# Performance work log

Hardware: AMD Instinct MI355X
Metric: run time of the kernel (lower is better)

The kernel has to match this reference:

```python
import jax, jax.numpy as jnp
import numpy as np

FACTOR = 5      # ProbAttention sampling factor
NHEAD = 8
LN_EPS = 1e-5


def pos_encoding(L, d):
    pos = np.arange(L, dtype=np.float32)[:, None]
    div = np.exp(np.arange(0, d, 2, dtype=np.float32) * (-np.log(10000.0) / d))
    pe = np.zeros((L, d), np.float32)
    pe[:, 0::2] = np.sin(pos * div)
    pe[:, 1::2] = np.cos(pos * div)
    return jnp.asarray(pe)


def layer_norm(x, s, b):
    mu = x.mean(-1, keepdims=True)
    var = ((x - mu) ** 2).mean(-1, keepdims=True)
    return (x - mu) * jax.lax.rsqrt(var + LN_EPS) * s + b


def prob_attention(x4, key):
    # x4: [B, L, H, D]; self-attention (Q=K=V=x4), mask_flag=False
    B, L, H, D = x4.shape
    q = jnp.transpose(x4, (0, 2, 1, 3))  # [B,H,L,D]
    u = max(1, min(FACTOR * int(np.ceil(np.log(L))), L))  # L_Q == L_K
    # random K-sampling: per-query random subset of keys (shared across B,H)
    idx = jax.random.randint(key, (L, u), 0, L)
    k_s = q[:, :, idx, :]                                # [B,H,L,u,D] irregular gather
    qk_s = jnp.einsum('bhld,bhlsd->bhls', q, k_s)        # [B,H,L,u]
    M = qk_s.max(-1) - qk_s.sum(-1) / L                  # sparsity measure
    _, top = jax.lax.top_k(M, u)                         # [B,H,u] active queries
    q_red = jnp.take_along_axis(q, top[..., None], axis=2)   # [B,H,u,D]
    scale = 1.0 / jnp.sqrt(jnp.float32(D))
    scores = jnp.einsum('bhud,bhkd->bhuk', q_red, q) * scale  # reduced-query scores
    attn = jax.nn.softmax(scores, axis=-1)
    ctx_top = jnp.einsum('bhuk,bhkd->bhud', attn, q)     # V == q here
    # initial context = mean of V (mask_flag=False), scatter top-query results
    ctx = jnp.broadcast_to(q.mean(axis=2, keepdims=True), (B, H, L, D))
    bi = jnp.arange(B)[:, None, None]
    hi = jnp.arange(H)[None, :, None]
    ctx = ctx.at[bi, hi, top].set(ctx_top)
    return jnp.transpose(ctx, (0, 2, 1, 3))  # [B,L,H,D]


def encoder_layer(x4, ln1_s, ln1_b, w1, b1, w2, b2, ln2_s, ln2_b, key):
    B, L, H, D = x4.shape
    new = prob_attention(x4, key)
    x = x4.reshape(B, L, H * D)
    x = layer_norm(x + new.reshape(B, L, H * D), ln1_s, ln1_b)
    # conv1/conv2 with kernel_size=1 == pointwise linears
    y = jax.nn.gelu(jnp.einsum('bld,fd->blf', x, w1) + b1, approximate=False)
    y = jnp.einsum('blf,df->bld', y, w2) + b2
    x = layer_norm(x + y, ln2_s, ln2_b)
    return x.reshape(B, L, H, D)


def distil(x4, factor=2):
    # DistilledAttention: mean-pool over `factor` timesteps (zero-pad to multiple)
    B, L, H, D = x4.shape
    pad = (-L) % factor
    if pad:
        x4 = jnp.pad(x4, ((0, 0), (0, pad), (0, 0), (0, 0)))
    return x4.reshape(B, -1, factor, H, D).mean(axis=2)


def setup_inputs() -> dict:
    key = jax.random.key(0)
    B, L, IN, D, DF, NL = 8, 4096, 64, 512, 2048, 3
    ks = jax.random.split(key, 16)
    s = 0.02
    return {
        'x': jax.random.normal(ks[0], (B, L, IN), jnp.float32),
        'emb_w': jax.random.normal(ks[1], (D, IN), jnp.float32) * s,
        'emb_b': jnp.zeros((D,), jnp.float32),
        'ln1_s': jnp.ones((NL, D), jnp.float32),
        'ln1_b': jnp.zeros((NL, D), jnp.float32),
        'w1': jax.random.normal(ks[2], (NL, DF, D), jnp.float32) * s,
        'b1': jnp.zeros((NL, DF), jnp.float32),
        'w2': jax.random.normal(ks[3], (NL, D, DF), jnp.float32) * s,
        'b2': jnp.zeros((NL, D), jnp.float32),
        'ln2_s': jnp.ones((NL, D), jnp.float32),
        'ln2_b': jnp.zeros((NL, D), jnp.float32),
        'out_w': jax.random.normal(ks[4], (D, D), jnp.float32) * s,
        'out_b': jnp.zeros((D,), jnp.float32),
    }


def reference(x, emb_w, emb_b, ln1_s, ln1_b, w1, b1, w2, b2, ln2_s, ln2_b, out_w, out_b):
    B, L, _ = x.shape
    D = emb_w.shape[0]
    hd = D // NHEAD
    h = jnp.einsum('bli,di->bld', x, emb_w) + emb_b
    h = h + pos_encoding(L, D)[None]
    h = h.reshape(B, L, NHEAD, hd)
    NL = ln1_s.shape[0]
    rkey = jax.random.key(42)  # deterministic ProbSparse sampling
    for i in range(NL):
        h = encoder_layer(h, ln1_s[i], ln1_b[i], w1[i], b1[i], w2[i], b2[i],
                          ln2_s[i], ln2_b[i], jax.random.fold_in(rkey, i))
        if i < NL - 1:
            h = distil(h)
    B2, L2 = h.shape[:2]
    h = h.reshape(B2, L2, D)
    return jnp.einsum('bld,od->blo', h, out_w) + out_b
```

## Files before the change

### kernel.cpp

```cpp
#include <hip/hip_runtime.h>
#include <hip/hip_bf16.h>
#include <math.h>


typedef short short8 __attribute__((ext_vector_type(8)));
typedef float f32x4 __attribute__((ext_vector_type(4)));
typedef unsigned int uint;

__host__ __device__ inline void tf2x32(unsigned k0, unsigned k1,
                                       unsigned x0, unsigned x1,
                                       unsigned& o0, unsigned& o1) {
  unsigned ks2 = k0 ^ k1 ^ 0x1BD11BDAu;
#define TF_R(x, r) x0 += x1; x1 = ((x1 << (r)) | (x1 >> (32 - (r)))); x1 ^= x0;
  x0 += k0; x1 += k1;
  TF_R(x1,13) TF_R(x1,15) TF_R(x1,26) TF_R(x1,6)
  x0 += k1; x1 += ks2 + 1u;
  TF_R(x1,17) TF_R(x1,29) TF_R(x1,16) TF_R(x1,24)
  x0 += ks2; x1 += k0 + 2u;
  TF_R(x1,13) TF_R(x1,15) TF_R(x1,26) TF_R(x1,6)
  x0 += k0; x1 += k1 + 3u;
  TF_R(x1,17) TF_R(x1,29) TF_R(x1,16) TF_R(x1,24)
  x0 += k1; x1 += ks2 + 4u;
  TF_R(x1,13) TF_R(x1,15) TF_R(x1,26) TF_R(x1,6)
  x0 += ks2; x1 += k0 + 5u;
#undef TF_R
  o0 = x0; o1 = x1;
}


__device__ inline unsigned bsplit(float x, float y, float& rx, float& ry) {
  union { __hip_bfloat162 h; unsigned u; } c;
  c.h = __float22bfloat162_rn(make_float2(x, y));
  rx = x - __uint_as_float(c.u << 16);
  ry = y - __uint_as_float(c.u & 0xffff0000u);
  return c.u;
}

__device__ inline void split2u(float4 v0, float4 v1, uint4& H, uint4& M) {
  float r[8]; float d0, d1;
  H.x = bsplit(v0.x, v0.y, r[0], r[1]);
  H.y = bsplit(v0.z, v0.w, r[2], r[3]);
  H.z = bsplit(v1.x, v1.y, r[4], r[5]);
  H.w = bsplit(v1.z, v1.w, r[6], r[7]);
  M.x = bsplit(r[0], r[1], d0, d1);
  M.y = bsplit(r[2], r[3], d0, d1);
  M.z = bsplit(r[4], r[5], d0, d1);
  M.w = bsplit(r[6], r[7], d0, d1);
}

__global__ void k_idx(int* __restrict__ idx, unsigned k2a, unsigned k2b,
                      int n, int mask) {
  int j = blockIdx.x * 256 + threadIdx.x;
  if (j >= n) return;
  unsigned o0, o1;
  tf2x32(k2a, k2b, 0u, (unsigned)j, o0, o1);
  idx[j] = (int)((o0 ^ o1) & (unsigned)mask);
}

__global__ __launch_bounds__(256) void k_pe(float* __restrict__ pe) {
  int d2 = threadIdx.x;
  int l0 = blockIdx.x * 16;
  double th = exp((double)(2 * d2) * (-9.210340371976184 / 512.0));
  double sT = sin(th), cT = cos(th);
  double a = (double)l0 * th;
  double s = sin(a), c = cos(a);
  float* row = pe + (size_t)l0 * 512 + 2 * d2;
#pragma unroll
  for (int i = 0; i < 16; i++) {
    row[0] = (float)s; row[1] = (float)c;
    double ns = s * cT + c * sT;
    double nc = c * cT - s * sT;
    s = ns; c = nc;
    row += 512;
  }
}

__global__ __launch_bounds__(256) void k_embed(const float* __restrict__ x,
    const float* __restrict__ W, const float* __restrict__ eb,
    const float* __restrict__ pe, float* __restrict__ out) {
  __shared__ __align__(16) float xs[16][64];
  int r0 = blockIdx.x * 16;
  int t = threadIdx.x;
  ((float4*)&xs[0][0])[t] = ((const float4*)(x + (size_t)r0 * 64))[t];
  __syncthreads();
  int d0 = t, d1 = t + 256;
  float acc0[16], acc1[16];
#pragma unroll
  for (int r = 0; r < 16; r++) { acc0[r] = 0.f; acc1[r] = 0.f; }
  for (int k = 0; k < 64; k++) {
    float w0 = W[d0 * 64 + k], w1 = W[d1 * 64 + k];
#pragma unroll
    for (int r = 0; r < 16; r++) {
      float xv = xs[r][k];
      acc0[r] = fmaf(xv, w0, acc0[r]);
      acc1[r] = fmaf(xv, w1, acc1[r]);
    }
  }
  float eb0 = eb[d0], eb1 = eb[d1];
#pragma unroll
  for (int r = 0; r < 16; r++) {
    int row = r0 + r;
    int l = row & 4095;
    out[(size_t)row * 512 + d0] = acc0[r] + eb0 + pe[(size_t)l * 512 + d0];
    out[(size_t)row * 512 + d1] = acc1[r] + eb1 + pe[(size_t)l * 512 + d1];
  }
}

__global__ __launch_bounds__(256) void k_colmean1(const float* __restrict__ X,
    double* __restrict__ part, int L, int S) {
  int seg = blockIdx.x, bh = blockIdx.y, b = bh >> 3, h = bh & 7;
  int w = threadIdx.x >> 6, d = threadIdx.x & 63;
  int rows = L / S, r0 = seg * rows;
  const float* base = X + (size_t)b * L * 512 + h * 64 + d;
  double s = 0.0;
  for (int l = r0 + w; l < r0 + rows; l += 4) s += (double)base[(size_t)l * 512];
  __shared__ double red[4][64];
  red[w][d] = s;
  __syncthreads();
  if (w == 0)
    part[((size_t)bh * S + seg) * 64 + d] =
        red[0][d] + red[1][d] + red[2][d] + red[3][d];
}

__global__ void k_colmean2(const double* __restrict__ part,
    float* __restrict__ meanq, int L, int S) {
  int bh = blockIdx.x, d = threadIdx.x;
  const double* p = part + (size_t)bh * S * 64 + d;
  double s = 0.0;
  for (int seg = 0; seg < S; seg++) s += p[seg * 64];
  meanq[bh * 64 + d] = (float)(s / (double)L);
}

__global__ __launch_bounds__(256) void k_M(const float* __restrict__ X,
    const int* __restrict__ idx, float* __restrict__ Mout, int L, int Lsh,
    int u, float invL) {
  int w = threadIdx.x >> 6, lane = threadIdx.x & 63;
  int gl = blockIdx.x * 4 + w;
  int l = gl & (L - 1), bh = gl >> Lsh, b = bh >> 3, h = bh & 7;
  const float* Xbh = X + (size_t)b * L * 512 + h * 64;
  __shared__ float qs[4][64];
  qs[w][lane] = Xbh[(size_t)l * 512 + lane];
  __syncthreads();
  const int s16 = lane >> 2, j = lane & 3;
  float4 qv[4];
#pragma unroll
  for (int c = 0; c < 4; c++) qv[c] = *(const float4*)&qs[w][c * 16 + j * 4];
  const int base = l * u;
  int kx[3];
#pragma unroll
  for (int g = 0; g < 3; g++) {
    int s = g * 16 + s16;
    kx[g] = (s < u) ? idx[base + s] : 0;
  }
  float4 kv[3][4];
#pragma unroll
  for (int g = 0; g < 3; g++) {
    const float* row = Xbh + (size_t)kx[g] * 512 + j * 4;
#pragma unroll
    for (int c = 0; c < 4; c++) kv[g][c] = *(const float4*)(row + c * 16);
  }
  float mv = -1e30f, sv = 0.f;
#pragma unroll
  for (int g = 0; g < 3; g++) {
    float pc[4];
#pragma unroll
    for (int c = 0; c < 4; c++) {
      float p = qv[c].x * kv[g][c].x;
      p = fmaf(qv[c].y, kv[g][c].y, p);
      p = fmaf(qv[c].z, kv[g][c].z, p);
      p = fmaf(qv[c].w, kv[g][c].w, p);
      pc[c] = p;
    }
    float d = (pc[0] + pc[1]) + (pc[2] + pc[3]);
    d += __shfl_xor(d, 1);
    d += __shfl_xor(d, 2);
    if (g * 16 + s16 < u) { mv = fmaxf(mv, d); sv += d; }
  }
  for (int off = 4; off < 64; off <<= 1) {
    mv = fmaxf(mv, __shfl_xor(mv, off));
    sv += __shfl_xor(sv, off);
  }
  if (lane == 0) Mout[(size_t)bh * L + l] = mv - sv * invL;
}

__global__ __launch_bounds__(256) void k_topk(const float* __restrict__ M,
    int* __restrict__ top, int L, int u) {
  __shared__ float mv[4096];
  __shared__ float wv[4];
  __shared__ int wi[4];
  __shared__ int bi_s;
  int bh = blockIdx.x, t = threadIdx.x;
  int w = t >> 6, lane = t & 63;
  const float* Mr = M + (size_t)bh * L;
  for (int k = t; k < L; k += 256) mv[k] = Mr[k];
  __syncthreads();
  float lv = -1e30f; int li = 0x7fffffff;
  for (int k = t; k < L; k += 256) {
    float v = mv[k];
    if (v > lv) { lv = v; li = k; }
  }
  for (int it = 0; it < u; it++) {
    float v = lv; int i = li;
#pragma unroll
    for (int off = 1; off < 64; off <<= 1) {
      float v2 = __shfl_xor(v, off); int i2 = __shfl_xor(i, off);
      if (v2 > v || (v2 == v && i2 < i)) { v = v2; i = i2; }
    }
    if (lane == 0) { wv[w] = v; wi[w] = i; }
    __syncthreads();
    if (t == 0) {
      float bv = wv[0]; int bi = wi[0];
#pragma unroll
      for (int jj = 1; jj < 4; jj++) {
        if (wv[jj] > bv || (wv[jj] == bv && wi[jj] < bi)) { bv = wv[jj]; bi = wi[jj]; }
      }
      top[bh * u + it] = bi;
      mv[bi] = -1e30f;
      bi_s = bi;
    }
    __syncthreads();
    int bi = bi_s;
    if ((bi & 255) == t) {
      lv = -1e30f; li = 0x7fffffff;
      for (int k = t; k < L; k += 256) {
        float v = mv[k];
        if (v > lv) { lv = v; li = k; }
      }
    }
  }
}

__global__ __launch_bounds__(256) void k_scores(const float* __restrict__ X,
    const int* __restrict__ top, float* __restrict__ S, int L, int u) {
  __shared__ __align__(16) float ktT[64][68];
  __shared__ __align__(16) float qred[48][64];
  int bh = blockIdx.y, b = bh >> 3, h = bh & 7;
  int k0 = blockIdx.x * 64;
  int t = threadIdx.x;
  const float* Xbh = X + (size_t)b * L * 512 + h * 64;
#pragma unroll
  for (int it = 0; it < 4; it++) {
    int lin = t + it * 256;
    int kk = lin >> 4, fi = lin & 15;
    float4 v = *(const float4*)(Xbh + (size_t)(k0 + kk) * 512 + fi * 4);
    ktT[fi * 4 + 0][kk] = v.x; ktT[fi * 4 + 1][kk] = v.y;
    ktT[fi * 4 + 2][kk] = v.z; ktT[fi * 4 + 3][kk] = v.w;
  }
#pragma unroll
  for (int it = 0; it < 3; it++) {
    int lin = t + it * 256;
    int ur = lin >> 4, fi = lin & 15;
    if (ur < u) {
      int row = top[bh * u + ur];
      *(float4*)(&qred[ur][fi * 4]) = *(const float4*)(Xbh + (size_t)row * 512 + fi * 4);
    } else if (ur < 48) {
      *(float4*)(&qred[ur][fi * 4]) = make_float4(0.f, 0.f, 0.f, 0.f);
    }
  }
  __syncthreads();
  int xq = t & 15, y = t >> 4;
  float acc[3][4];
#pragma unroll
  for (int j = 0; j < 3; j++)
#pragma unroll
    for (int e = 0; e < 4; e++) acc[j][e] = 0.f;
  for (int d = 0; d < 64; d++) {
    float4 kv = *(const float4*)(&ktT[d][xq * 4]);
#pragma unroll
    for (int j = 0; j < 3; j++) {
      float qv = qred[y * 3 + j][d];
      acc[j][0] = fmaf(qv, kv.x, acc[j][0]);
      acc[j][1] = fmaf(qv, kv.y, acc[j][1]);
      acc[j][2] = fmaf(qv, kv.z, acc[j][2]);
      acc[j][3] = fmaf(qv, kv.w, acc[j][3]);
    }
  }
#pragma unroll
  for (int j = 0; j < 3; j++) {
    int ur = y * 3 + j;
    if (ur < u) {
      float4 o = make_float4(acc[j][0] * 0.125f, acc[j][1] * 0.125f,
                             acc[j][2] * 0.125f, acc[j][3] * 0.125f);
      *(float4*)(S + ((size_t)(bh * u + ur)) * L + k0 + xq * 4) = o;
    }
  }
}

#define PVSEG 8
__global__ __launch_bounds__(256) void k_pv(const float* __restrict__ X,
    const float* __restrict__ S, float* __restrict__ P2,
    float* __restrict__ MS, float* __restrict__ SS, int L, int u) {
  __shared__ __align__(16) float xs[32][64];
  __shared__ __align__(16) float wsm[32][52];
  int seg = blockIdx.x, bh = blockIdx.y, b = bh >> 3, h = bh & 7;
  int t = threadIdx.x, w = t >> 6, lane = t & 63;
  int rows = L / PVSEG, l0 = seg * rows;
  const float* Xb = X + (size_t)b * L * 512 + h * 64;
  int li = lane & 31, par = lane >> 5;
  const float* Sp[6]; int val[6];
#pragma unroll
  for (int jj = 0; jj < 6; jj++) {
    int ur = w * 12 + par + jj * 2;
    val[jj] = (ur < u);
    Sp[jj] = S + (size_t)(bh * u + (val[jj] ? ur : 0)) * L + l0 + li;
  }
  float mloc[6];
#pragma unroll
  for (int jj = 0; jj < 6; jj++) mloc[jj] = -1e30f;
  for (int c = 0; c < rows; c += 32) {
#pragma unroll
    for (int jj = 0; jj < 6; jj++) mloc[jj] = fmaxf(mloc[jj], Sp[jj][c]);
  }
#pragma unroll
  for (int jj = 0; jj < 6; jj++) {
#pragma unroll
    for (int off = 1; off < 32; off <<= 1)
      mloc[jj] = fmaxf(mloc[jj], __shfl_xor(mloc[jj], off));
  }
  float acc[12], esum[6];
#pragma unroll
  for (int j = 0; j < 12; j++) acc[j] = 0.f;
#pragma unroll
  for (int j = 0; j < 6; j++) esum[j] = 0.f;
  int xr = t >> 4, xf = t & 15;
  for (int c = 0; c < rows; c += 32) {
    __syncthreads();
    *(float4*)&xs[xr][xf * 4] =
        *(const float4*)(Xb + (size_t)(l0 + c + xr) * 512 + xf * 4);
    *(float4*)&xs[16 + xr][xf * 4] =
        *(const float4*)(Xb + (size_t)(l0 + c + 16 + xr) * 512 + xf * 4);
#pragma unroll
    for (int jj = 0; jj < 6; jj++) {
      float e = val[jj] ? expf(Sp[jj][c] - mloc[jj]) : 0.f;
      esum[jj] += e;
      wsm[li][w * 12 + par + jj * 2] = e;
    }
    __syncthreads();
#pragma unroll 2
    for (int l = 0; l < 32; l++) {
      float xv = xs[l][lane];
      float4 w0 = *(const float4*)&wsm[l][w * 12];
      float4 w1 = *(const float4*)&wsm[l][w * 12 + 4];
      float4 w2 = *(const float4*)&wsm[l][w * 12 + 8];
      acc[0]  = fmaf(w0.x, xv, acc[0]);  acc[1]  = fmaf(w0.y, xv, acc[1]);
      acc[2]  = fmaf(w0.z, xv, acc[2]);  acc[3]  = fmaf(w0.w, xv, acc[3]);
      acc[4]  = fmaf(w1.x, xv, acc[4]);  acc[5]  = fmaf(w1.y, xv, acc[5]);
      acc[6]  = fmaf(w1.z, xv, acc[6]);  acc[7]  = fmaf(w1.w, xv, acc[7]);
      acc[8]  = fmaf(w2.x, xv, acc[8]);  acc[9]  = fmaf(w2.y, xv, acc[9]);
      acc[10] = fmaf(w2.z, xv, acc[10]); acc[11] = fmaf(w2.w, xv, acc[11]);
    }
  }
  float* P = P2 + ((size_t)(bh * PVSEG + seg) * 48 + w * 12) * 64 + lane;
#pragma unroll
  for (int j = 0; j < 12; j++) P[j * 64] = acc[j];
#pragma unroll
  for (int jj = 0; jj < 6; jj++) {
    float es = esum[jj];
#pragma unroll
    for (int off = 1; off < 32; off <<= 1) es += __shfl_xor(es, off);
    if (li == 0) {
      int ur = w * 12 + par + jj * 2;
      MS[((size_t)bh * PVSEG + seg) * 48 + ur] = mloc[jj];
      SS[((size_t)bh * PVSEG + seg) * 48 + ur] = es;
    }
  }
}

__global__ __launch_bounds__(256) void k_pvred(const float* __restrict__ P2,
    const float* __restrict__ MS, const float* __restrict__ SS,
    const int* __restrict__ top, float* __restrict__ CTX,
    char* __restrict__ FLG, int L, int u) {
  int bh = blockIdx.x;
  int t = threadIdx.x;
  const float* Pb = P2 + (size_t)bh * PVSEG * 48 * 64;
  const float* Mb = MS + (size_t)bh * PVSEG * 48;
  const float* Sb = SS + (size_t)bh * PVSEG * 48;
  __shared__ float fac[PVSEG][48];
  __shared__ double dens[48];
  if (t < u) {
    float mx = Mb[t];
#pragma unroll
    for (int s = 1; s < PVSEG; s++) mx = fmaxf(mx, Mb[s * 48 + t]);
    double den = 0.0;
#pragma unroll
    for (int s = 0; s < PVSEG; s++) {
      float f = expf(Mb[s * 48 + t] - mx);
      fac[s][t] = f;
      den += (double)Sb[s * 48 + t] * (double)f;
    }
    dens[t] = den;
  }
  __syncthreads();
  for (int e = t; e < u * 64; e += 256) {
    int ur = e >> 6, d = e & 63;
    const float* p = Pb + ur * 64 + d;
    const int st = 48 * 64;
    double num = 0.0;
#pragma unroll
    for (int s = 0; s < PVSEG; s++)
      num += (double)p[s * st] * (double)fac[s][ur];
    double tot = num / dens[ur];
    CTX[((size_t)bh * 48 + ur) * 64 + d] = (float)tot;
    if (d == 0) FLG[(size_t)bh * L + top[bh * u + ur]] = (char)(ur + 1);
  }
}

__global__ __launch_bounds__(256) void k_ln1(float* __restrict__ X,
    const char* __restrict__ FLG, const float* __restrict__ CTX,
    const float* __restrict__ meanq, const float* __restrict__ gs,
    const float* __restrict__ gb, char* __restrict__ XPbase, int L, int Lsh) {
  int w = threadIdx.x >> 6, lane = threadIdx.x & 63;
  int row = blockIdx.x * 4 + w;
  int b = row >> Lsh, l = row & (L - 1);
  float* xr = X + (size_t)row * 512;
  int h = lane >> 3;
  int bh = b * 8 + h;
  int flag = (int)FLG[(size_t)bh * L + l];
  float4 c0, c1;
  if (flag) {
    const float* cx = CTX + ((size_t)bh * 48 + (flag - 1)) * 64 + (lane & 7) * 8;
    c0 = *(const float4*)cx; c1 = *(const float4*)(cx + 4);
  } else {
    const float* mq = meanq + b * 512 + lane * 8;
    c0 = *(const float4*)mq; c1 = *(const float4*)(mq + 4);
  }
  float4 x0 = *(const float4*)(xr + lane * 8);
  float4 x1 = *(const float4*)(xr + lane * 8 + 4);
  float v[8] = { x0.x + c0.x, x0.y + c0.y, x0.z + c0.z, x0.w + c0.w,
                 x1.x + c1.x, x1.y + c1.y, x1.z + c1.z, x1.w + c1.w };
  double s = 0.0, s2 = 0.0;
#pragma unroll
  for (int i = 0; i < 8; i++) { s += (double)v[i]; s2 += (double)v[i] * (double)v[i]; }
  for (int off = 32; off; off >>= 1) { s += __shfl_xor(s, off); s2 += __shfl_xor(s2, off); }
  double mu = s * (1.0 / 512.0);
  double var = s2 * (1.0 / 512.0) - mu * mu;
  float rsd = (float)(1.0 / sqrt(var + 1e-5));
  float muf = (float)mu;
  float4 g0 = *(const float4*)(gs + lane * 8);
  float4 g1 = *(const float4*)(gs + lane * 8 + 4);
  float4 b0 = *(const float4*)(gb + lane * 8);
  float4 b1 = *(const float4*)(gb + lane * 8 + 4);
  float4 y0 = make_float4((v[0] - muf) * rsd * g0.x + b0.x,
                          (v[1] - muf) * rsd * g0.y + b0.y,
                          (v[2] - muf) * rsd * g0.z + b0.z,
                          (v[3] - muf) * rsd * g0.w + b0.w);
  float4 y1 = make_float4((v[4] - muf) * rsd * g1.x + b1.x,
                          (v[5] - muf) * rsd * g1.y + b1.y,
                          (v[6] - muf) * rsd * g1.z + b1.z,
                          (v[7] - muf) * rsd * g1.w + b1.w);
  *(float4*)(xr + lane * 8) = y0;
  *(float4*)(xr + lane * 8 + 4) = y1;
  int c = row >> 13, ml = row & 8191;
  char* P = XPbase + ((size_t)c << 24);
  const size_t psz = (size_t)8192 * 512 * 2;
  int k = lane * 8;
  size_t off = ((size_t)(ml >> 4) * 16 + (k >> 5)) * 1024
             + (size_t)(((k >> 3) & 3) * 256 + (ml & 15) * 16);
  uint4 H, Md;
  split2u(y0, y1, H, Md);
  *(uint4*)(P + off) = H;
  *(uint4*)(P + psz + off) = Md;
}

__global__ __launch_bounds__(256) void k_ln2(const float* __restrict__ X,
    const float* __restrict__ Y2, const float* __restrict__ gs,
    const float* __restrict__ gb, float* __restrict__ out) {
  int w = threadIdx.x >> 6, lane = threadIdx.x & 63;
  int orow = blockIdx.x * 4 + w;
  float o[8] = {0.f,0.f,0.f,0.f,0.f,0.f,0.f,0.f};
  for (int p = 0; p < 2; p++) {
    int row = orow * 2 + p;
    const float* xr = X + (size_t)row * 512;
    const float* yr = Y2 + (size_t)row * 512;
    float v[8]; double s = 0.0, s2 = 0.0;
#pragma unroll
    for (int i = 0; i < 8; i++) {
      float val = xr[lane + i * 64] + yr[lane + i * 64];
      v[i] = val; s += (double)val; s2 += (double)val * (double)val;
    }
    for (int off = 32; off; off >>= 1) { s += __shfl_xor(s, off); s2 += __shfl_xor(s2, off); }
    double mu = s * (1.0 / 512.0);
    double var = s2 * (1.0 / 512.0) - mu * mu;
    float rsd = (float)(1.0 / sqrt(var + 1e-5));
    float muf = (float)mu;
#pragma unroll
    for (int i = 0; i < 8; i++)
      o[i] += (v[i] - muf) * rsd * gs[lane + i * 64] + gb[lane + i * 64];
  }
#pragma unroll
  for (int i = 0; i < 8; i++)
    out[(size_t)orow * 512 + lane + i * 64] = o[i] * 0.5f;
}

__global__ __launch_bounds__(256) void k_ln2p(const float* __restrict__ X,
    const float* __restrict__ Y2, const float* __restrict__ gs,
    const float* __restrict__ gb, char* __restrict__ P) {
  int w = threadIdx.x >> 6, lane = threadIdx.x & 63;
  int row = blockIdx.x * 4 + w;
  const float* xr = X + (size_t)row * 512;
  const float* yr = Y2 + (size_t)row * 512;
  float4 x0 = *(const float4*)(xr + lane * 8);
  float4 x1 = *(const float4*)(xr + lane * 8 + 4);
  float4 z0 = *(const float4*)(yr + lane * 8);
  float4 z1 = *(const float4*)(yr + lane * 8 + 4);
  float v[8] = { x0.x + z0.x, x0.y + z0.y, x0.z + z0.z, x0.w + z0.w,
                 x1.x + z1.x, x1.y + z1.y, x1.z + z1.z, x1.w + z1.w };
  double s = 0.0, s2 = 0.0;
#pragma unroll
  for (int i = 0; i < 8; i++) { s += (double)v[i]; s2 += (double)v[i] * (double)v[i]; }
  for (int off = 32; off; off >>= 1) { s += __shfl_xor(s, off); s2 += __shfl_xor(s2, off); }
  double mu = s * (1.0 / 512.0);
  double var = s2 * (1.0 / 512.0) - mu * mu;
  float rsd = (float)(1.0 / sqrt(var + 1e-5));
  float muf = (float)mu;
  float4 g0 = *(const float4*)(gs + lane * 8);
  float4 g1 = *(const float4*)(gs + lane * 8 + 4);
  float4 b0 = *(const float4*)(gb + lane * 8);
  float4 b1 = *(const float4*)(gb + lane * 8 + 4);
  float4 y0 = make_float4((v[0] - muf) * rsd * g0.x + b0.x,
                          (v[1] - muf) * rsd * g0.y + b0.y,
                          (v[2] - muf) * rsd * g0.z + b0.z,
                          (v[3] - muf) * rsd * g0.w + b0.w);
  float4 y1 = make_float4((v[4] - muf) * rsd * g1.x + b1.x,
                          (v[5] - muf) * rsd * g1.y + b1.y,
                          (v[6] - muf) * rsd * g1.z + b1.z,
                          (v[7] - muf) * rsd * g1.w + b1.w);
  const size_t psz = (size_t)8192 * 512 * 2;
  int k = lane * 8;
  size_t off = ((size_t)(row >> 4) * 16 + (k >> 5)) * 1024
             + (size_t)(((k >> 3) & 3) * 256 + (row & 15) * 16);
  uint4 H, Md;
  split2u(y0, y1, H, Md);
  *(uint4*)(P + off) = H;
  *(uint4*)(P + psz + off) = Md;
}

__global__ void k_splitX(const float* __restrict__ X, char* __restrict__ P,
                         int K, int total8) {
  int f = blockIdx.x * 256 + threadIdx.x;
  if (f >= total8) return;
  int k8 = f % (K >> 3), m = f / (K >> 3);
  int k = k8 * 8;
  const float* src = X + (size_t)m * K + k;
  float4 v0 = *(const float4*)(src);
  float4 v1 = *(const float4*)(src + 4);
  uint4 H, Md;
  split2u(v0, v1, H, Md);
  size_t psz = (size_t)total8 * 16;
  size_t off = ((size_t)(m >> 4) * (K >> 5) + (k >> 5)) * 1024
             + (size_t)(((k >> 3) & 3) * 256 + (m & 15) * 16);
  *(uint4*)(P + off) = H;
  *(uint4*)(P + psz + off) = Md;
}

__device__ __forceinline__ void async16(void* lds, const void* g) {
  __builtin_amdgcn_global_load_lds(
      (const __attribute__((address_space(1))) uint*)g,
      (__attribute__((address_space(3))) uint*)lds, 16, 0, 0);
}

template <int MT, int GELU, int PLANES_OUT>
__global__ __launch_bounds__(256) void k_gemm6(const char* __restrict__ AP,
    const char* __restrict__ BP, const float* __restrict__ bias,
    void* __restrict__ Cout, int N, int K) {
  __shared__ __align__(16) char lds[(MT * 2 + 16) * 1024];
  const int t = threadIdx.x;
  const int w = t >> 6, lane = t & 63;
  int lin = blockIdx.y * gridDim.x + blockIdx.x;
  const int nb = gridDim.x * gridDim.y;
  lin = (lin & 7) * (nb >> 3) + (lin >> 3);
  const int shx = 31 - __clz(gridDim.x);
  const int bx = lin & (gridDim.x - 1), by = lin >> shx;
  const int quad = lane >> 4, rit = lane & 15;
  const int Mrows = gridDim.y * (MT * 16);
  const size_t psA = (size_t)Mrows * K * 2;
  const size_t psB = (size_t)N * K * 2;
  const int KB = K >> 5;
  char* ldsA = lds;
  char* ldsB = lds + MT * 2 * 1024;
  const int wm = (w >> 1) * (MT / 2), wn = (w & 1) * 4;
  f32x4 acc[MT / 2][4];
#pragma unroll
  for (int i = 0; i < MT / 2; i++)
#pragma unroll
    for (int j = 0; j < 4; j++) acc[i][j] = (f32x4){0.f, 0.f, 0.f, 0.f};
  for (int kt = 0; kt < KB; kt++) {
#pragma unroll
    for (int r = 0; r < MT / 2; r++) {
      int q = w + 4 * r;
      int p = q / MT, tt = q % MT;
      async16(ldsA + (p * MT + tt) * 1024,
              AP + p * psA + ((size_t)(by * MT + tt) * KB + kt) * 1024 + lane * 16);
    }
#pragma unroll
    for (int r = 0; r < 4; r++) {
      int q = w + 4 * r;
      int p = q >> 3, tt = q & 7;
      async16(ldsB + (p * 8 + tt) * 1024,
              BP + p * psB + ((size_t)(bx * 8 + tt) * KB + kt) * 1024 + lane * 16);
    }
    __syncthreads();
    short8 af[2][MT / 2];
#pragma unroll
    for (int p = 0; p < 2; p++)
#pragma unroll
      for (int mi = 0; mi < MT / 2; mi++)
        af[p][mi] = *(const short8*)(ldsA + (p * MT + wm + mi) * 1024 + lane * 16);
#pragma unroll
    for (int ni = 0; ni < 4; ni++) {
      const char* bb = ldsB + (wn + ni) * 1024 + lane * 16;
      short8 bh = *(const short8*)(bb);
      short8 bm = *(const short8*)(bb + 8192);
#pragma unroll
      for (int mi = 0; mi < MT / 2; mi++) {
        f32x4 c = acc[mi][ni];
        c = __builtin_amdgcn_mfma_f32_16x16x32_bf16(af[0][mi], bh, c, 0, 0, 0);
        c = __builtin_amdgcn_mfma_f32_16x16x32_bf16(af[0][mi], bm, c, 0, 0, 0);
        c = __builtin_amdgcn_mfma_f32_16x16x32_bf16(af[1][mi], bh, c, 0, 0, 0);
        acc[mi][ni] = c;
      }
    }
    __syncthreads();
  }
  const int n0 = bx * 128, m_base = by * (MT * 16);
  if (!PLANES_OUT) {
    float* C = (float*)Cout;
#pragma unroll
    for (int mi = 0; mi < MT / 2; mi++) {
      const int gr0 = m_base + (wm + mi) * 16 + quad * 4;
#pragma unroll
      for (int ni = 0; ni < 4; ni++) {
        const int gc = n0 + (wn + ni) * 16 + rit;
        const float bia = bias[gc];
#pragma unroll
        for (int e = 0; e < 4; e++) {
          float v = acc[mi][ni][e] + bia;
          if (GELU) v = 0.5f * v * (1.0f + erff(v * 0.7071067811865476f));
          C[(size_t)(gr0 + e) * N + gc] = v;
        }
      }
    }
  } else {
    char* CP = (char*)Cout;
    const size_t psC = (size_t)Mrows * N * 2;
    float* lf = (float*)lds;
    for (int h = 0; h < 2; h++) {
      __syncthreads();
      if ((w & 1) == h) {
#pragma unroll
        for (int ni = 0; ni < 4; ni++) {
          const float bia = bias[n0 + h * 64 + ni * 16 + rit];
#pragma unroll
          for (int mi = 0; mi < MT / 2; mi++) {
            const int ml0 = (wm + mi) * 16 + quad * 4;
#pragma unroll
            for (int e = 0; e < 4; e++) {
              float v = acc[mi][ni][e] + bia;
              if (GELU) v = 0.5f * v * (1.0f + erff(v * 0.7071067811865476f));
              lf[(ml0 + e) * 64 + ni * 16 + rit] = v;
            }
          }
        }
      }
      __syncthreads();
#pragma unroll
      for (int it = 0; it < (MT * 16 * 8) / 256; it++) {
        int p = it * 256 + t;
        int ml = p >> 3, n8 = p & 7;
        float4 v0 = *(const float4*)&lf[ml * 64 + n8 * 8];
        float4 v1 = *(const float4*)&lf[ml * 64 + n8 * 8 + 4];
        uint4 H, Md;
        split2u(v0, v1, H, Md);
        int mg = m_base + ml, kg = n0 + h * 64 + n8 * 8;
        size_t off = ((size_t)(mg >> 4) * (N >> 5) + (kg >> 5)) * 1024
                   + (size_t)(((kg >> 3) & 3) * 256 + (mg & 15) * 16);
        *(uint4*)(CP + off) = H;
        *(uint4*)(CP + psC + off) = Md;
      }
    }
  }
}

extern "C" void kernel_launch(void* const* d_in, const int* in_sizes, int n_in,
                              void* d_out, int out_size, void* d_ws, size_t ws_size,
                              hipStream_t stream) {
  const float* x     = (const float*)d_in[0];
  const float* emb_w = (const float*)d_in[1];
  const float* emb_b = (const float*)d_in[2];
  const float* ln1_s = (const float*)d_in[3];
  const float* ln1_b = (const float*)d_in[4];
  const float* w1    = (const float*)d_in[5];
  const float* b1    = (const float*)d_in[6];
  const float* w2    = (const float*)d_in[7];
  const float* b2    = (const float*)d_in[8];
  const float* ln2_s = (const float*)d_in[9];
  const float* ln2_b = (const float*)d_in[10];
  const float* out_w = (const float*)d_in[11];
  const float* out_b = (const float*)d_in[12];
  float* outp = (float*)d_out;

  char* ws = (char*)d_ws;
  if (ws_size < (212ULL << 20)) return;
  float* PE    = (float*)(ws);
  char*  W1S   = ws;
  float* BUF[3] = { (float*)(ws + (8ULL << 20)),
                    (float*)(ws + (72ULL << 20)),
                    (float*)(ws + (136ULL << 20)) };
  char*  W2S   = ws + (200ULL << 20);
  float* MB    = (float*)(ws + (206ULL << 20));
  int*   IDX   = (int*)  (ws + (207ULL << 20));
  int*   TOP   = (int*)  (ws + (208ULL << 20));
  float* MEANQ = (float*)(ws + (208ULL << 20) + (64 << 10));
  double* PART = (double*)(ws + (209ULL << 20));
  char*  FLG   = ws + (210ULL << 20);
  float* CTX   = (float*)(ws + (210ULL << 20) + (512 << 10));

  k_pe<<<256, 256, 0, stream>>>(PE);
  k_embed<<<(8 * 4096) / 16, 256, 0, stream>>>(x, emb_w, emb_b, PE, BUF[0]);

  const int Ls[3] = {4096, 2048, 1024};
  const int Lshs[3] = {12, 11, 10};
  const int us[3] = {45, 40, 35};
  int xi = 0, ai = 1, yi = 2;
  char* FINALP = nullptr;
  for (int layer = 0; layer < 3; layer++) {
    const int L = Ls[layer], u = us[layer];
    float* X = BUF[xi]; float* A = BUF[ai]; float* Y = BUF[yi];

    k_splitX<<<(2048 * 512 / 8) / 256, 256, 0, stream>>>(
        w1 + (size_t)layer * 2048 * 512, W1S, 512, 2048 * 512 / 8);
    k_splitX<<<(512 * 2048 / 8) / 256, 256, 0, stream>>>(
        w2 + (size_t)layer * 512 * 2048, W2S, 2048, 512 * 2048 / 8);

    unsigned Ka, Kb, k2a, k2b;
    tf2x32(0u, 42u, 0u, (unsigned)layer, Ka, Kb);
    tf2x32(Ka, Kb, 0u, 1u, k2a, k2b);
    const int n = L * u;
    k_idx<<<(n + 255) / 256, 256, 0, stream>>>(IDX, k2a, k2b, n, L - 1);
    const int S = 32;
    k_colmean1<<<dim3(S, 64), 256, 0, stream>>>(X, PART, L, S);
    k_colmean2<<<64, 64, 0, stream>>>(PART, MEANQ, L, S);
    k_M<<<64 * L / 4, 256, 0, stream>>>(X, IDX, MB, L, Lshs[layer], u,
                                        1.0f / (float)L);
    k_topk<<<64, 256, 0, stream>>>(MB, TOP, L, u);
    hipMemsetAsync(FLG, 0, (size_t)64 * L, stream);
    float* P2 = (float*)((char*)Y + (48ULL << 20));
    float* MS = (float*)((char*)Y + (56ULL << 20));
    float* SS = (float*)((char*)Y + (57ULL << 20));
    k_scores<<<dim3(L / 64, 64), 256, 0, stream>>>(X, TOP, Y, L, u);
    k_pv<<<dim3(PVSEG, 64), 256, 0, stream>>>(X, Y, P2, MS, SS, L, u);
    k_pvred<<<64, 256, 0, stream>>>(P2, MS, SS, TOP, CTX, FLG, L, u);
    k_ln1<<<8 * L / 4, 256, 0, stream>>>(X, FLG, CTX, MEANQ,
                                         ln1_s + layer * 512,
                                         ln1_b + layer * 512, (char*)A,
                                         L, Lshs[layer]);

    char* YP = (char*)Y;
    const int chunks = (8 * L) / 8192;
    for (int c = 0; c < chunks; c++) {
      float* Ac = A + (size_t)c * 8192 * 512;
      char* XP = (char*)Ac;
      k_gemm6<8, 1, 1><<<dim3(16, 64), 256, 0, stream>>>(
          XP, W1S, b1 + layer * 2048, YP, 2048, 512);
      k_gemm6<4, 0, 0><<<dim3(4, 128), 256, 0, stream>>>(
          YP, W2S, b2 + layer * 512, Ac, 512, 2048);
    }
    if (layer < 2) {
      k_ln2<<<8 * (L / 2) / 4, 256, 0, stream>>>(X, A, ln2_s + layer * 512,
                                                 ln2_b + layer * 512, Y);
    } else {
      FINALP = (char*)Y;
      k_ln2p<<<8 * L / 4, 256, 0, stream>>>(X, A, ln2_s + layer * 512,
                                            ln2_b + layer * 512, FINALP);
    }
    int tswap = xi; xi = yi; yi = ai; ai = tswap;
  }
  char* WOS = W2S;
  k_splitX<<<(512 * 512 / 8) / 256, 256, 0, stream>>>(out_w, WOS, 512, 512 * 512 / 8);
  k_gemm6<4, 0, 0><<<dim3(4, 128), 256, 0, stream>>>(
      FINALP, WOS, out_b, outp, 512, 512);
}
```

Baseline: 2.074 ms.

## Double-buffer LDS in bf16 split GEMM with async prefetch two tiles ahead

The GEMM kernel now keeps two LDS buffers and issues async global-to-LDS loads for tile kt+2 while MFMAs run on the current tile. Explicit vmcnt waits and raw barriers replace the two __syncthreads per iteration, and wave priority is raised around the MFMA block. The aim is to hide global load latency behind compute. In exchange LDS use per block doubles, which may lower occupancy, and correctness now depends on the hand-tuned waitcnt values.

```diff
diff --git a/kernel.cpp b/kernel.cpp
--- a/kernel.cpp
+++ b/kernel.cpp
@@ -563,7 +563,8 @@
 __global__ __launch_bounds__(256) void k_gemm6(const char* __restrict__ AP,
     const char* __restrict__ BP, const float* __restrict__ bias,
     void* __restrict__ Cout, int N, int K) {
-  __shared__ __align__(16) char lds[(MT * 2 + 16) * 1024];
+  constexpr int NT = MT * 2 + 16;
+  __shared__ __align__(16) char lds[2 * NT * 1024];
   const int t = threadIdx.x;
   const int w = t >> 6, lane = t & 63;
   int lin = blockIdx.y * gridDim.x + blockIdx.x;
@@ -576,52 +577,80 @@
   const size_t psA = (size_t)Mrows * K * 2;
   const size_t psB = (size_t)N * K * 2;
   const int KB = K >> 5;
-  char* ldsA = lds;
-  char* ldsB = lds + MT * 2 * 1024;
   const int wm = (w >> 1) * (MT / 2), wn = (w & 1) * 4;
-  f32x4 acc[MT / 2][4];
-#pragma unroll
-  for (int i = 0; i < MT / 2; i++)
-#pragma unroll
-    for (int j = 0; j < 4; j++) acc[i][j] = (f32x4){0.f, 0.f, 0.f, 0.f};
-  for (int kt = 0; kt < KB; kt++) {
+
+  auto STAGE = [&](char* buf, int kt) {
+    char* bufA = buf;
+    char* bufB = buf + MT * 2 * 1024;
 #pragma unroll
     for (int r = 0; r < MT / 2; r++) {
       int q = w + 4 * r;
       int p = q / MT, tt = q % MT;
-      async16(ldsA + (p * MT + tt) * 1024,
+      async16(bufA + (p * MT + tt) * 1024,
               AP + p * psA + ((size_t)(by * MT + tt) * KB + kt) * 1024 + lane * 16);
     }
 #pragma unroll
     for (int r = 0; r < 4; r++) {
       int q = w + 4 * r;
       int p = q >> 3, tt = q & 7;
-      async16(ldsB + (p * 8 + tt) * 1024,
+      async16(bufB + (p * 8 + tt) * 1024,
               BP + p * psB + ((size_t)(bx * 8 + tt) * KB + kt) * 1024 + lane * 16);
     }
-    __syncthreads();
-    short8 af[2][MT / 2];
+  };
+
+  f32x4 acc[MT / 2][4];
+#pragma unroll
+  for (int i = 0; i < MT / 2; i++)
+#pragma unroll
+    for (int j = 0; j < 4; j++) acc[i][j] = (f32x4){0.f, 0.f, 0.f, 0.f};
+
+  STAGE(lds, 0);
+  STAGE(lds + NT * 1024, 1);
+  if constexpr (MT == 8) asm volatile("s_waitcnt vmcnt(8)" ::: "memory");
+  else                   asm volatile("s_waitcnt vmcnt(6)" ::: "memory");
+  __builtin_amdgcn_s_barrier();
+  __builtin_amdgcn_sched_barrier(0);
+
+  for (int kt = 0; kt < KB; kt++) {
+    char* cb = lds + (kt & 1) * (NT * 1024);
+    short8 af[2][MT / 2], bf[2][4];
 #pragma unroll
     for (int p = 0; p < 2; p++)
 #pragma unroll
       for (int mi = 0; mi < MT / 2; mi++)
-        af[p][mi] = *(const short8*)(ldsA + (p * MT + wm + mi) * 1024 + lane * 16);
+        af[p][mi] = *(const short8*)(cb + (p * MT + wm + mi) * 1024 + lane * 16);
 #pragma unroll
     for (int ni = 0; ni < 4; ni++) {
-      const char* bb = ldsB + (wn + ni) * 1024 + lane * 16;
-      short8 bh = *(const short8*)(bb);
-      short8 bm = *(const short8*)(bb + 8192);
+      const char* bb = cb + MT * 2 * 1024 + (wn + ni) * 1024 + lane * 16;
+      bf[0][ni] = *(const short8*)(bb);
+      bf[1][ni] = *(const short8*)(bb + 8192);
+    }
+    asm volatile("s_waitcnt lgkmcnt(0)" ::: "memory");
+    __builtin_amdgcn_sched_barrier(0);
+    __builtin_amdgcn_s_barrier();
+    if (kt + 2 < KB) STAGE(cb, kt + 2);
+    __builtin_amdgcn_s_setprio(1);
+#pragma unroll
+    for (int ni = 0; ni < 4; ni++)
 #pragma unroll
       for (int mi = 0; mi < MT / 2; mi++) {
         f32x4 c = acc[mi][ni];
-        c = __builtin_amdgcn_mfma_f32_16x16x32_bf16(af[0][mi], bh, c, 0, 0, 0);
-        c = __builtin_amdgcn_mfma_f32_16x16x32_bf16(af[0][mi], bm, c, 0, 0, 0);
-        c = __builtin_amdgcn_mfma_f32_16x16x32_bf16(af[1][mi], bh, c, 0, 0, 0);
+        c = __builtin_amdgcn_mfma_f32_16x16x32_bf16(af[0][mi], bf[0][ni], c, 0, 0, 0);
+        c = __builtin_amdgcn_mfma_f32_16x16x32_bf16(af[0][mi], bf[1][ni], c, 0, 0, 0);
+        c = __builtin_amdgcn_mfma_f32_16x16x32_bf16(af[1][mi], bf[0][ni], c, 0, 0, 0);
         acc[mi][ni] = c;
       }
-    }
-    __syncthreads();
-  }
+    __builtin_amdgcn_s_setprio(0);
+    if (kt + 2 < KB) {
+      if constexpr (MT == 8) asm volatile("s_waitcnt vmcnt(8)" ::: "memory");
+      else                   asm volatile("s_waitcnt vmcnt(6)" ::: "memory");
+    } else {
+      asm volatile("s_waitcnt vmcnt(0)" ::: "memory");
+    }
+    __builtin_amdgcn_s_barrier();
+    __builtin_amdgcn_sched_barrier(0);
+  }
+
   const int n0 = bx * 128, m_base = by * (MT * 16);
   if (!PLANES_OUT) {
     float* C = (float*)Cout;
```

Result: faster. 2.016 ms, median of 2 (-2.8%).
